# Performance work log

Measured on AMD Instinct MI355X. Metric: run time of the kernel, lower is better.

Reference implementation:

```python
import jax, jax.numpy as jnp
import numpy as np

N, E, DIM, H = 50000, 800000, 64, 2
HD = H * DIM


def setup_inputs() -> dict:
    key = jax.random.key(0)
    ks = jax.random.split(key, 16)
    s = 0.05
    return {
        "x": jax.random.normal(ks[0], (N, DIM), jnp.float32),
        "edge_index": jax.random.randint(ks[1], (2, E), 0, N, jnp.int64),
        "Wq": jax.random.normal(ks[2], (DIM, HD), jnp.float32) * s,
        "bq": jax.random.normal(ks[3], (HD,), jnp.float32) * s,
        "Wk": jax.random.normal(ks[4], (DIM, HD), jnp.float32) * s,
        "bk": jax.random.normal(ks[5], (HD,), jnp.float32) * s,
        "Wv": jax.random.normal(ks[6], (DIM, HD), jnp.float32) * s,
        "bv": jax.random.normal(ks[7], (HD,), jnp.float32) * s,
        "Wskip": jax.random.normal(ks[8], (DIM, HD), jnp.float32) * s,
        "bskip": jax.random.normal(ks[9], (HD,), jnp.float32) * s,
        "Wc": jax.random.normal(ks[10], (HD, DIM), jnp.float32) * s,
        "bc": jax.random.normal(ks[11], (DIM,), jnp.float32) * s,
        "gamma": jnp.ones((DIM,), jnp.float32),
        "beta": jnp.zeros((DIM,), jnp.float32),
    }


def reference(x, edge_index, Wq, bq, Wk, bk, Wv, bv, Wskip, bskip, Wc, bc, gamma, beta):
    src, dst = edge_index[0], edge_index[1]  # messages flow src -> dst
    # TransformerConv: per-head q/k/v projections, [N, H, D]
    q = (x @ Wq + bq).reshape(N, H, DIM)
    k = (x @ Wk + bk).reshape(N, H, DIM)
    v = (x @ Wv + bv).reshape(N, H, DIM)
    scale = 1.0 / np.sqrt(DIM).astype(np.float32)
    # edge-wise attention logits: [E, H]
    alpha = jnp.einsum('ehd,ehd->eh', q[dst], k[src]) * scale
    # segment softmax over incoming edges of each dst node (PyG softmax)
    amax = jax.ops.segment_max(alpha, dst, num_segments=N)
    a = jnp.exp(alpha - amax[dst])
    asum = jax.ops.segment_sum(a, dst, num_segments=N)
    a = a / (asum[dst] + 1e-16)
    # weighted scatter-aggregate of values: [N, H, D] -> concat heads
    out = jax.ops.segment_sum(a[:, :, None] * v[src], dst, num_segments=N)
    out = out.reshape(N, HD)
    # root/skip connection (root_weight=True default)
    out = out + (x @ Wskip + bskip)
    # concat linear: H*D -> dim
    out = out @ Wc + bc
    # pyg.LayerNorm default mode='graph': normalize over ALL nodes+features
    out = out - out.mean()
    out = out / (out.std() + 1e-5)  # std with unbiased=False (jnp default ddof=0)
    return out * gamma + beta
```

## Files before the change

### kernel.cpp

```cpp
#include <hip/hip_runtime.h>
#include <hip/hip_bf16.h>

#define N_NODES 50000
#define N_EDGES 800000
#define DIM 64
#define NHEAD 2
#define HD 128
#define NCOL 448
#define MAXDEG 64

#define NBIN 196
#define BCAP 6144
#define ACH 2048
#define BIN_BLKS 391

#define PREP_B 112
#define PROJ_B 782

#define QSCALE 0.18033688011112042f

typedef short bf16x8 __attribute__((ext_vector_type(8)));
typedef float f32x16 __attribute__((ext_vector_type(16)));
typedef float f32x2 __attribute__((ext_vector_type(2)));

__device__ __forceinline__ unsigned short f2bf(float f) {
    unsigned u = __float_as_uint(f);
    unsigned r = (u + 0x7fffu + ((u >> 16) & 1u)) >> 16;
    return (unsigned short)r;
}
__device__ __forceinline__ unsigned char f2fp8(float f) {
    int r = __builtin_amdgcn_cvt_pk_fp8_f32(f, f, 0, false);
    return (unsigned char)(r & 0xff);
}

__global__ __launch_bounds__(256) void k_pb(
    const int* __restrict__ ei,
    const float* __restrict__ Wq, const float* __restrict__ bq,
    const float* __restrict__ Wk, const float* __restrict__ bk,
    const float* __restrict__ Wv, const float* __restrict__ bv,
    const float* __restrict__ Wskip, const float* __restrict__ bskip,
    const float* __restrict__ Wc, const float* __restrict__ bc,
    unsigned short* __restrict__ WallT, float* __restrict__ ball,
    int* __restrict__ bincnt, unsigned* __restrict__ bins,
    double* __restrict__ stats)
{
    const int t = threadIdx.x;
    if (blockIdx.x < PREP_B) {
        int gid = blockIdx.x * 256 + t;
        if (gid == 0) { stats[0] = 0.0; stats[1] = 0.0; }
        const int j = gid >> 6;
        const int d = gid & 63;
        float w, bb;
        if (j < 128) {
            w = Wq[d * HD + j] * QSCALE;
            bb = bq[j] * QSCALE;
        } else if (j < 256) {
            int jj = j - 128;
            w = Wk[d * HD + jj];
            bb = bk[jj];
        } else if (j < 384) {
            int jj = j - 256;
            int h = jj >> 6, jc = jj & 63;
            float s = 0.f, sb = 0.f;
            for (int c = 0; c < 64; c++) {
                float wc = Wc[(h * 64 + c) * DIM + jc];
                s  += Wv[d * HD + h * 64 + c] * wc;
                sb += bv[h * 64 + c] * wc;
            }
            w = s; bb = sb;
        } else {
            int jj = j - 384;
            float s = 0.f, sb = bc[jj];
            for (int c = 0; c < HD; c++) {
                float wc = Wc[c * DIM + jj];
                s  += Wskip[d * HD + c] * wc;
                sb += bskip[c] * wc;
            }
            w = s; bb = sb;
        }
        WallT[gid] = f2bf(w);
        if (d == 0) ball[j] = bb;
        return;
    }
    __shared__ unsigned pk[ACH];
    __shared__ unsigned char bbn[ACH];
    __shared__ unsigned ord[ACH];
    __shared__ int hist[256];
    __shared__ int lofs[256];
    __shared__ int gbase[256];
    const int e0 = (blockIdx.x - PREP_B) * ACH;
    hist[t] = 0;
    __syncthreads();
    for (int i = t; i < ACH; i += 256) {
        int e = e0 + i;
        if (e < N_EDGES) {
            int src = ei[e];
            int d = ei[N_EDGES + e];
            int bin = d >> 8;
            pk[i] = (unsigned)(((d & 255) << 16) | src);
            bbn[i] = (unsigned char)bin;
            atomicAdd(&hist[bin], 1);
        } else {
            bbn[i] = 255;
        }
    }
    __syncthreads();
    int h = hist[t];
    lofs[t] = h;
    __syncthreads();
    for (int off = 1; off < 256; off <<= 1) {
        int add = (t >= off) ? lofs[t - off] : 0;
        __syncthreads();
        lofs[t] += add;
        __syncthreads();
    }
    int excl = lofs[t] - h;
    if (t < NBIN && h > 0) gbase[t] = atomicAdd(&bincnt[t], h);
    __syncthreads();
    lofs[t] = excl;
    hist[t] = 0;
    __syncthreads();
    for (int i = t; i < ACH; i += 256) {
        int bin = bbn[i];
        if (bin != 255) {
            int sl = atomicAdd(&hist[bin], 1);
            ord[lofs[bin] + sl] = pk[i];
        }
    }
    __syncthreads();
    const int w = t >> 6, lane = t & 63;
    for (int bin = w; bin < NBIN; bin += 4) {
        int cnt = hist[bin];
        int lo = lofs[bin];
        int gb = gbase[bin];
        for (int i = lane; i < cnt; i += 64) {
            int pos = gb + i;
            if (pos < BCAP) bins[(size_t)bin * BCAP + pos] = ord[lo + i];
        }
    }
}

__global__ __launch_bounds__(256) void k_ep(
    const float* __restrict__ x,
    const unsigned short* __restrict__ WallT, const float* __restrict__ ball,
    float* __restrict__ q, unsigned char* __restrict__ kv, float* __restrict__ skipc,
    const int* __restrict__ bincnt, const unsigned* __restrict__ bins,
    int* __restrict__ deg, unsigned short* __restrict__ elist)
{
    const int blk = blockIdx.x;
    const int t = threadIdx.x;
    if (blk >= PROJ_B) {
        const int bin = blk - PROJ_B;
        __shared__ int nodecnt[256];
        nodecnt[t] = 0;
        __syncthreads();
        int cnt = bincnt[bin]; if (cnt > BCAP) cnt = BCAP;
        const unsigned* bp = bins + (size_t)bin * BCAP;
        for (int i = t; i < cnt; i += 256) {
            unsigned p = bp[i];
            int local = p >> 16;
            int src = p & 0xffff;
            int sl = atomicAdd(&nodecnt[local], 1);
            if (sl < MAXDEG)
                elist[((size_t)((bin << 8) | local)) * MAXDEG + sl] = (unsigned short)src;
        }
        __syncthreads();
        int node = (bin << 8) + t;
        if (node < N_NODES) {
            int dgv = nodecnt[t];
            deg[node] = dgv > MAXDEG ? MAXDEG : dgv;
        }
        return;
    }
    const int w = t >> 6;
    const int lane = t & 63;
    const int col = lane & 31;
    const int khalf = lane >> 5;
    const int n0 = blk * 64 + (w >> 1) * 32;
    const int ct0 = (w & 1) * 7;
    const int rowbase = 4 * khalf;

    int nread = n0 + col; if (nread >= N_NODES) nread = N_NODES - 1;
    const float* ap = x + (size_t)nread * 64 + khalf * 8;
    bf16x8 afrag[4];
#pragma unroll
    for (int kk = 0; kk < 4; kk++) {
        float4 xa = *((const float4*)(ap + kk * 16));
        float4 xb4 = *((const float4*)(ap + kk * 16 + 4));
        bf16x8 f;
        f[0] = (short)f2bf(xa.x); f[1] = (short)f2bf(xa.y);
        f[2] = (short)f2bf(xa.z); f[3] = (short)f2bf(xa.w);
        f[4] = (short)f2bf(xb4.x); f[5] = (short)f2bf(xb4.y);
        f[6] = (short)f2bf(xb4.z); f[7] = (short)f2bf(xb4.w);
        afrag[kk] = f;
    }

    for (int tt = 0; tt < 7; tt++) {
        const int gc = (ct0 + tt) * 32 + col;
        const float b = ball[gc];
        f32x16 acc;
#pragma unroll
        for (int r = 0; r < 16; r++) acc[r] = b;
        const unsigned short* bp = WallT + (size_t)gc * 64 + khalf * 8;
#pragma unroll
        for (int kk = 0; kk < 4; kk++) {
            bf16x8 bfrag = *((const bf16x8*)(bp + kk * 16));
            acc = __builtin_amdgcn_mfma_f32_32x32x16_bf16(afrag[kk], bfrag, acc, 0, 0, 0);
        }
        if (gc < 128) {
#pragma unroll
            for (int r = 0; r < 16; r++) {
                int node = n0 + (r & 3) + 8 * (r >> 2) + rowbase;
                if (node < N_NODES) q[(size_t)node * HD + gc] = acc[r];
            }
        } else if (gc < 384) {
            int ch = gc - 128;
#pragma unroll
            for (int r = 0; r < 16; r++) {
                int node = n0 + (r & 3) + 8 * (r >> 2) + rowbase;
                if (node < N_NODES) kv[(size_t)node * 256 + ch] = f2fp8(acc[r]);
            }
        } else {
#pragma unroll
            for (int r = 0; r < 16; r++) {
                int node = n0 + (r & 3) + 8 * (r >> 2) + rowbase;
                if (node < N_NODES) skipc[(size_t)node * DIM + (gc - 384)] = acc[r];
            }
        }
    }
}

__global__ __launch_bounds__(256) void k_attn(
    const float* __restrict__ q, const unsigned char* __restrict__ kv,
    const float* __restrict__ skipc,
    const int* __restrict__ deg, const unsigned short* __restrict__ elist,
    float* __restrict__ out, float* __restrict__ parts)
{
    const int w = threadIdx.x >> 6;
    const int lane = threadIdx.x & 63;
    const int g = lane >> 3;
    const int j = lane & 7;
    const int n = blockIdx.x * 4 + w;
    const f32x2* qp = (const f32x2*)(q + (size_t)n * HD);
    f32x2 q0[4], q1[4];
#pragma unroll
    for (int i = 0; i < 4; i++) { q0[i] = qp[4 * j + i]; q1[i] = qp[32 + 4 * j + i]; }
    const int myE = elist[(size_t)n * MAXDEG + lane];
    f32x2 acc0[4], acc1[4];
#pragma unroll
    for (int i = 0; i < 4; i++) {
        acc0[i] = (f32x2){0.f, 0.f};
        acc1[i] = (f32x2){0.f, 0.f};
    }
    float l0 = 0.f, l1 = 0.f;
    int dg = deg[n]; if (dg > MAXDEG) dg = MAXDEG;
    for (int b0 = 0; b0 < dg; b0 += 16) {
        int iA = b0 + g, iB = b0 + 8 + g;
        bool vA = iA < dg, vB = iB < dg;
        int sA = __shfl(myE, vA ? iA : 0, 64);
        int sB = __shfl(myE, vB ? iB : 0, 64);
        const uint2* kpA = (const uint2*)(kv + (size_t)sA * 256);
        const uint2* kpB = (const uint2*)(kv + (size_t)sB * 256);
        uint2 KA0 = kpA[j],      KA1 = kpA[8 + j];
        uint2 VA0 = kpA[16 + j], VA1 = kpA[24 + j];
        uint2 KB0 = kpB[j],      KB1 = kpB[8 + j];
        uint2 VB0 = kpB[16 + j], VB1 = kpB[24 + j];
        f32x2 pa0 = q0[0] * __builtin_amdgcn_cvt_pk_f32_fp8(KA0.x, false);
        pa0 += q0[1] * __builtin_amdgcn_cvt_pk_f32_fp8(KA0.x, true);
        pa0 += q0[2] * __builtin_amdgcn_cvt_pk_f32_fp8(KA0.y, false);
        pa0 += q0[3] * __builtin_amdgcn_cvt_pk_f32_fp8(KA0.y, true);
        f32x2 pa1 = q1[0] * __builtin_amdgcn_cvt_pk_f32_fp8(KA1.x, false);
        pa1 += q1[1] * __builtin_amdgcn_cvt_pk_f32_fp8(KA1.x, true);
        pa1 += q1[2] * __builtin_amdgcn_cvt_pk_f32_fp8(KA1.y, false);
        pa1 += q1[3] * __builtin_amdgcn_cvt_pk_f32_fp8(KA1.y, true);
        float p0A = pa0[0] + pa0[1];
        float p1A = pa1[0] + pa1[1];
        f32x2 pb0 = q0[0] * __builtin_amdgcn_cvt_pk_f32_fp8(KB0.x, false);
        pb0 += q0[1] * __builtin_amdgcn_cvt_pk_f32_fp8(KB0.x, true);
        pb0 += q0[2] * __builtin_amdgcn_cvt_pk_f32_fp8(KB0.y, false);
        pb0 += q0[3] * __builtin_amdgcn_cvt_pk_f32_fp8(KB0.y, true);
        f32x2 pb1 = q1[0] * __builtin_amdgcn_cvt_pk_f32_fp8(KB1.x, false);
        pb1 += q1[1] * __builtin_amdgcn_cvt_pk_f32_fp8(KB1.x, true);
        pb1 += q1[2] * __builtin_amdgcn_cvt_pk_f32_fp8(KB1.y, false);
        pb1 += q1[3] * __builtin_amdgcn_cvt_pk_f32_fp8(KB1.y, true);
        float p0B = pb0[0] + pb0[1];
        float p1B = pb1[0] + pb1[1];
#pragma unroll
        for (int off = 1; off < 8; off <<= 1) {
            p0A += __shfl_xor(p0A, off, 64);
            p1A += __shfl_xor(p1A, off, 64);
            p0B += __shfl_xor(p0B, off, 64);
            p1B += __shfl_xor(p1B, off, 64);
        }
        float w0A = vA ? __builtin_amdgcn_exp2f(p0A) : 0.f;
        float w1A = vA ? __builtin_amdgcn_exp2f(p1A) : 0.f;
        float w0B = vB ? __builtin_amdgcn_exp2f(p0B) : 0.f;
        float w1B = vB ? __builtin_amdgcn_exp2f(p1B) : 0.f;
        l0 += w0A + w0B; l1 += w1A + w1B;
        f32x2 w0Av = {w0A, w0A}, w1Av = {w1A, w1A};
        f32x2 w0Bv = {w0B, w0B}, w1Bv = {w1B, w1B};
        acc0[0] += w0Av * __builtin_amdgcn_cvt_pk_f32_fp8(VA0.x, false);
        acc0[1] += w0Av * __builtin_amdgcn_cvt_pk_f32_fp8(VA0.x, true);
        acc0[2] += w0Av * __builtin_amdgcn_cvt_pk_f32_fp8(VA0.y, false);
        acc0[3] += w0Av * __builtin_amdgcn_cvt_pk_f32_fp8(VA0.y, true);
        acc1[0] += w1Av * __builtin_amdgcn_cvt_pk_f32_fp8(VA1.x, false);
        acc1[1] += w1Av * __builtin_amdgcn_cvt_pk_f32_fp8(VA1.x, true);
        acc1[2] += w1Av * __builtin_amdgcn_cvt_pk_f32_fp8(VA1.y, false);
        acc1[3] += w1Av * __builtin_amdgcn_cvt_pk_f32_fp8(VA1.y, true);
        acc0[0] += w0Bv * __builtin_amdgcn_cvt_pk_f32_fp8(VB0.x, false);
        acc0[1] += w0Bv * __builtin_amdgcn_cvt_pk_f32_fp8(VB0.x, true);
        acc0[2] += w0Bv * __builtin_amdgcn_cvt_pk_f32_fp8(VB0.y, false);
        acc0[3] += w0Bv * __builtin_amdgcn_cvt_pk_f32_fp8(VB0.y, true);
        acc1[0] += w1Bv * __builtin_amdgcn_cvt_pk_f32_fp8(VB1.x, false);
        acc1[1] += w1Bv * __builtin_amdgcn_cvt_pk_f32_fp8(VB1.x, true);
        acc1[2] += w1Bv * __builtin_amdgcn_cvt_pk_f32_fp8(VB1.y, false);
        acc1[3] += w1Bv * __builtin_amdgcn_cvt_pk_f32_fp8(VB1.y, true);
    }
    float* a0 = (float*)acc0;
    float* a1 = (float*)acc1;
#pragma unroll
    for (int off = 8; off < 64; off <<= 1) {
        l0 += __shfl_xor(l0, off, 64);
        l1 += __shfl_xor(l1, off, 64);
#pragma unroll
        for (int i = 0; i < 8; i++) {
            a0[i] += __shfl_xor(a0[i], off, 64);
            a1[i] += __shfl_xor(a1[i], off, 64);
        }
    }
    if (g == 0) {
        float inv0 = 1.f / (l0 + 1e-16f), inv1 = 1.f / (l1 + 1e-16f);
        const float4* sk = (const float4*)(skipc + (size_t)n * DIM);
        float4 sa = sk[2 * j], sb = sk[2 * j + 1];
        float o[8];
        o[0] = a0[0] * inv0 + a1[0] * inv1 + sa.x;
        o[1] = a0[1] * inv0 + a1[1] * inv1 + sa.y;
        o[2] = a0[2] * inv0 + a1[2] * inv1 + sa.z;
        o[3] = a0[3] * inv0 + a1[3] * inv1 + sa.w;
        o[4] = a0[4] * inv0 + a1[4] * inv1 + sb.x;
        o[5] = a0[5] * inv0 + a1[5] * inv1 + sb.y;
        o[6] = a0[6] * inv0 + a1[6] * inv1 + sb.z;
        o[7] = a0[7] * inv0 + a1[7] * inv1 + sb.w;
        float4 r0 = {o[0], o[1], o[2], o[3]}, r1 = {o[4], o[5], o[6], o[7]};
        float4* op = (float4*)(out + (size_t)n * DIM);
        op[2 * j] = r0; op[2 * j + 1] = r1;
        float s_ = 0.f, ss = 0.f;
#pragma unroll
        for (int i = 0; i < 8; i++) { s_ += o[i]; ss += o[i] * o[i]; }
#pragma unroll
        for (int off = 1; off < 8; off <<= 1) {
            s_ += __shfl_xor(s_, off, 64);
            ss += __shfl_xor(ss, off, 64);
        }
        if (j == 0) { parts[n] = s_; parts[N_NODES + n] = ss; }
    }
}

#define RED_BLOCKS 100
__global__ __launch_bounds__(256) void k_reduce(
    const float* __restrict__ parts, double* __restrict__ stats)
{
    double s = 0.0, ss = 0.0;
    for (int i = blockIdx.x * 256 + threadIdx.x; i < N_NODES; i += RED_BLOCKS * 256) {
        s  += (double)parts[i];
        ss += (double)parts[N_NODES + i];
    }
#pragma unroll
    for (int off = 32; off > 0; off >>= 1) {
        s  += __shfl_down(s, off);
        ss += __shfl_down(ss, off);
    }
    __shared__ double sdd[8];
    int wave = threadIdx.x >> 6;
    if ((threadIdx.x & 63) == 0) { sdd[wave * 2] = s; sdd[wave * 2 + 1] = ss; }
    __syncthreads();
    if (threadIdx.x == 0) {
        double S = 0.0, SS = 0.0;
        for (int w = 0; w < 4; w++) { S += sdd[w * 2]; SS += sdd[w * 2 + 1]; }
        atomicAdd(&stats[0], S);
        atomicAdd(&stats[1], SS);
    }
}

__global__ __launch_bounds__(256) void k_norm(
    float* __restrict__ out, const double* __restrict__ stats,
    const float* __restrict__ gamma, const float* __restrict__ beta)
{
    int i = blockIdx.x * 256 + threadIdx.x;
    if (i >= N_NODES * DIM / 4) return;
    const double cnt = (double)N_NODES * (double)DIM;
    double mean = stats[0] / cnt;
    double var  = stats[1] / cnt - mean * mean;
    if (var < 0.0) var = 0.0;
    float mf = (float)mean;
    float inv = 1.0f / ((float)sqrt(var) + 1e-5f);
    float4 v = ((const float4*)out)[i];
    float4 gv = ((const float4*)gamma)[i & 15];
    float4 bv2 = ((const float4*)beta)[i & 15];
    v.x = (v.x - mf) * inv * gv.x + bv2.x;
    v.y = (v.y - mf) * inv * gv.y + bv2.y;
    v.z = (v.z - mf) * inv * gv.z + bv2.z;
    v.w = (v.w - mf) * inv * gv.w + bv2.w;
    ((float4*)out)[i] = v;
}

extern "C" void kernel_launch(void* const* d_in, const int* in_sizes, int n_in,
                              void* d_out, int out_size, void* d_ws, size_t ws_size,
                              hipStream_t stream) {
    const float* x     = (const float*)d_in[0];
    const int*   ei    = (const int*)d_in[1];
    const float* Wq    = (const float*)d_in[2];
    const float* bq    = (const float*)d_in[3];
    const float* Wk    = (const float*)d_in[4];
    const float* bk    = (const float*)d_in[5];
    const float* Wv    = (const float*)d_in[6];
    const float* bv    = (const float*)d_in[7];
    const float* Wsk   = (const float*)d_in[8];
    const float* bsk   = (const float*)d_in[9];
    const float* Wc    = (const float*)d_in[10];
    const float* bc    = (const float*)d_in[11];
    const float* gamma = (const float*)d_in[12];
    const float* beta  = (const float*)d_in[13];
    float* out = (float*)d_out;

    float* ws = (float*)d_ws;
    const size_t NF = (size_t)N_NODES * HD;
    float* q = ws;
    unsigned char* kv = (unsigned char*)(ws + NF);
    float* skipc = (float*)(kv + (size_t)N_NODES * 256);
    unsigned short* WallT = (unsigned short*)(skipc + (size_t)N_NODES * DIM);
    float* ball   = (float*)(WallT + NCOL * 64);
    int* bincnt   = (int*)(ball + NCOL);
    unsigned* bins = (unsigned*)(bincnt + 256);
    int* deg      = (int*)(bins + (size_t)NBIN * BCAP);
    unsigned short* elist = (unsigned short*)(deg + N_NODES);
    float* parts  = (float*)(elist + (size_t)NBIN * 256 * MAXDEG);
    double* stats = (double*)(parts + (size_t)N_NODES * 2);

    hipMemsetAsync(bincnt, 0, NBIN * sizeof(int), stream);
    hipLaunchKernelGGL(k_pb, dim3(PREP_B + BIN_BLKS), dim3(256), 0, stream,
                       ei, Wq, bq, Wk, bk, Wv, bv, Wsk, bsk, Wc, bc,
                       WallT, ball, bincnt, bins, stats);
    hipLaunchKernelGGL(k_ep, dim3(PROJ_B + NBIN), dim3(256), 0, stream,
                       x, WallT, ball, q, kv, skipc, bincnt, bins, deg, elist);
    hipLaunchKernelGGL(k_attn, dim3(N_NODES / 4), dim3(256), 0, stream,
                       q, kv, skipc, deg, elist, out, parts);
    hipLaunchKernelGGL(k_reduce, dim3(RED_BLOCKS), dim3(256), 0, stream, parts, stats);
    hipLaunchKernelGGL(k_norm, dim3(N_NODES * DIM / 4 / 256 + 1), dim3(256), 0, stream,
                       out, stats, gamma, beta);
}
```

Measured before the change: 190.1 us.

## Replace two-pass binned edge bucketing with direct global-atomic adjacency build, interleave KV layout

The edge bucketing no longer sorts edges into bins in shared memory and then scatters them per bin in a second kernel. Each edge now does a global atomicAdd on its destination's degree and writes its source straight into that node's fixed-size adjacency slot. The K/V fp8 layout is interleaved so each lane fetches both heads' K and V with one 16-byte load per edge, and the attention loop now handles 8 edges per step instead of 16. The trade-off is many contended global atomics and scattered 2-byte writes in exchange for fewer kernel phases and no bin buffers. Degrees above MAXDEG are still clamped when read.

```diff
diff --git a/kernel.cpp b/kernel.cpp
--- a/kernel.cpp
+++ b/kernel.cpp
@@ -9,10 +9,8 @@
 #define NCOL 448
 #define MAXDEG 64
 
-#define NBIN 196
-#define BCAP 6144
 #define ACH 2048
-#define BIN_BLKS 391
+#define EDGE_BLKS 391
 
 #define PREP_B 112
 #define PROJ_B 782
@@ -41,7 +39,7 @@
     const float* __restrict__ Wskip, const float* __restrict__ bskip,
     const float* __restrict__ Wc, const float* __restrict__ bc,
     unsigned short* __restrict__ WallT, float* __restrict__ ball,
-    int* __restrict__ bincnt, unsigned* __restrict__ bins,
+    int* __restrict__ deg, unsigned short* __restrict__ elist,
     double* __restrict__ stats)
 {
     const int t = threadIdx.x;
@@ -82,60 +80,16 @@
         if (d == 0) ball[j] = bb;
         return;
     }
-    __shared__ unsigned pk[ACH];
-    __shared__ unsigned char bbn[ACH];
-    __shared__ unsigned ord[ACH];
-    __shared__ int hist[256];
-    __shared__ int lofs[256];
-    __shared__ int gbase[256];
     const int e0 = (blockIdx.x - PREP_B) * ACH;
-    hist[t] = 0;
-    __syncthreads();
+#pragma unroll 2
     for (int i = t; i < ACH; i += 256) {
         int e = e0 + i;
         if (e < N_EDGES) {
             int src = ei[e];
             int d = ei[N_EDGES + e];
-            int bin = d >> 8;
-            pk[i] = (unsigned)(((d & 255) << 16) | src);
-            bbn[i] = (unsigned char)bin;
-            atomicAdd(&hist[bin], 1);
-        } else {
-            bbn[i] = 255;
-        }
-    }
-    __syncthreads();
-    int h = hist[t];
-    lofs[t] = h;
-    __syncthreads();
-    for (int off = 1; off < 256; off <<= 1) {
-        int add = (t >= off) ? lofs[t - off] : 0;
-        __syncthreads();
-        lofs[t] += add;
-        __syncthreads();
-    }
-    int excl = lofs[t] - h;
-    if (t < NBIN && h > 0) gbase[t] = atomicAdd(&bincnt[t], h);
-    __syncthreads();
-    lofs[t] = excl;
-    hist[t] = 0;
-    __syncthreads();
-    for (int i = t; i < ACH; i += 256) {
-        int bin = bbn[i];
-        if (bin != 255) {
-            int sl = atomicAdd(&hist[bin], 1);
-            ord[lofs[bin] + sl] = pk[i];
-        }
-    }
-    __syncthreads();
-    const int w = t >> 6, lane = t & 63;
-    for (int bin = w; bin < NBIN; bin += 4) {
-        int cnt = hist[bin];
-        int lo = lofs[bin];
-        int gb = gbase[bin];
-        for (int i = lane; i < cnt; i += 64) {
-            int pos = gb + i;
-            if (pos < BCAP) bins[(size_t)bin * BCAP + pos] = ord[lo + i];
+            int sl = atomicAdd(&deg[d], 1);
+            if (sl < MAXDEG)
+                elist[(size_t)d * MAXDEG + sl] = (unsigned short)src;
         }
     }
 }
@@ -143,35 +97,10 @@
 __global__ __launch_bounds__(256) void k_ep(
     const float* __restrict__ x,
     const unsigned short* __restrict__ WallT, const float* __restrict__ ball,
-    float* __restrict__ q, unsigned char* __restrict__ kv, float* __restrict__ skipc,
-    const int* __restrict__ bincnt, const unsigned* __restrict__ bins,
-    int* __restrict__ deg, unsigned short* __restrict__ elist)
+    float* __restrict__ q, unsigned char* __restrict__ kv, float* __restrict__ skipc)
 {
     const int blk = blockIdx.x;
     const int t = threadIdx.x;
-    if (blk >= PROJ_B) {
-        const int bin = blk - PROJ_B;
-        __shared__ int nodecnt[256];
-        nodecnt[t] = 0;
-        __syncthreads();
-        int cnt = bincnt[bin]; if (cnt > BCAP) cnt = BCAP;
-        const unsigned* bp = bins + (size_t)bin * BCAP;
-        for (int i = t; i < cnt; i += 256) {
-            unsigned p = bp[i];
-            int local = p >> 16;
-            int src = p & 0xffff;
-            int sl = atomicAdd(&nodecnt[local], 1);
-            if (sl < MAXDEG)
-                elist[((size_t)((bin << 8) | local)) * MAXDEG + sl] = (unsigned short)src;
-        }
-        __syncthreads();
-        int node = (bin << 8) + t;
-        if (node < N_NODES) {
-            int dgv = nodecnt[t];
-            deg[node] = dgv > MAXDEG ? MAXDEG : dgv;
-        }
-        return;
-    }
     const int w = t >> 6;
     const int lane = t & 63;
     const int col = lane & 31;
@@ -215,10 +144,14 @@
             }
         } else if (gc < 384) {
             int ch = gc - 128;
+            int half = ch >> 7;
+            int cc = ch & 127;
+            int h = cc >> 6, c = cc & 63;
+            int pos = half * 128 + ((c >> 3) << 4) + (h << 3) + (c & 7);
 #pragma unroll
             for (int r = 0; r < 16; r++) {
                 int node = n0 + (r & 3) + 8 * (r >> 2) + rowbase;
-                if (node < N_NODES) kv[(size_t)node * 256 + ch] = f2fp8(acc[r]);
+                if (node < N_NODES) kv[(size_t)node * 256 + pos] = f2fp8(acc[r]);
             }
         } else {
 #pragma unroll
@@ -254,67 +187,40 @@
     }
     float l0 = 0.f, l1 = 0.f;
     int dg = deg[n]; if (dg > MAXDEG) dg = MAXDEG;
-    for (int b0 = 0; b0 < dg; b0 += 16) {
-        int iA = b0 + g, iB = b0 + 8 + g;
-        bool vA = iA < dg, vB = iB < dg;
-        int sA = __shfl(myE, vA ? iA : 0, 64);
-        int sB = __shfl(myE, vB ? iB : 0, 64);
-        const uint2* kpA = (const uint2*)(kv + (size_t)sA * 256);
-        const uint2* kpB = (const uint2*)(kv + (size_t)sB * 256);
-        uint2 KA0 = kpA[j],      KA1 = kpA[8 + j];
-        uint2 VA0 = kpA[16 + j], VA1 = kpA[24 + j];
-        uint2 KB0 = kpB[j],      KB1 = kpB[8 + j];
-        uint2 VB0 = kpB[16 + j], VB1 = kpB[24 + j];
-        f32x2 pa0 = q0[0] * __builtin_amdgcn_cvt_pk_f32_fp8(KA0.x, false);
-        pa0 += q0[1] * __builtin_amdgcn_cvt_pk_f32_fp8(KA0.x, true);
-        pa0 += q0[2] * __builtin_amdgcn_cvt_pk_f32_fp8(KA0.y, false);
-        pa0 += q0[3] * __builtin_amdgcn_cvt_pk_f32_fp8(KA0.y, true);
-        f32x2 pa1 = q1[0] * __builtin_amdgcn_cvt_pk_f32_fp8(KA1.x, false);
-        pa1 += q1[1] * __builtin_amdgcn_cvt_pk_f32_fp8(KA1.x, true);
-        pa1 += q1[2] * __builtin_amdgcn_cvt_pk_f32_fp8(KA1.y, false);
-        pa1 += q1[3] * __builtin_amdgcn_cvt_pk_f32_fp8(KA1.y, true);
-        float p0A = pa0[0] + pa0[1];
-        float p1A = pa1[0] + pa1[1];
-        f32x2 pb0 = q0[0] * __builtin_amdgcn_cvt_pk_f32_fp8(KB0.x, false);
-        pb0 += q0[1] * __builtin_amdgcn_cvt_pk_f32_fp8(KB0.x, true);
-        pb0 += q0[2] * __builtin_amdgcn_cvt_pk_f32_fp8(KB0.y, false);
-        pb0 += q0[3] * __builtin_amdgcn_cvt_pk_f32_fp8(KB0.y, true);
-        f32x2 pb1 = q1[0] * __builtin_amdgcn_cvt_pk_f32_fp8(KB1.x, false);
-        pb1 += q1[1] * __builtin_amdgcn_cvt_pk_f32_fp8(KB1.x, true);
-        pb1 += q1[2] * __builtin_amdgcn_cvt_pk_f32_fp8(KB1.y, false);
-        pb1 += q1[3] * __builtin_amdgcn_cvt_pk_f32_fp8(KB1.y, true);
-        float p0B = pb0[0] + pb0[1];
-        float p1B = pb1[0] + pb1[1];
+    for (int b0 = 0; b0 < dg; b0 += 8) {
+        int idx = b0 + g;
+        bool valid = idx < dg;
+        int s = __shfl(myE, valid ? idx : 0, 64);
+        const uint4* kp = (const uint4*)(kv + (size_t)s * 256);
+        uint4 K = kp[j];
+        uint4 V = kp[8 + j];
+        f32x2 p0v = q0[0] * __builtin_amdgcn_cvt_pk_f32_fp8(K.x, false);
+        p0v += q0[1] * __builtin_amdgcn_cvt_pk_f32_fp8(K.x, true);
+        p0v += q0[2] * __builtin_amdgcn_cvt_pk_f32_fp8(K.y, false);
+        p0v += q0[3] * __builtin_amdgcn_cvt_pk_f32_fp8(K.y, true);
+        f32x2 p1v = q1[0] * __builtin_amdgcn_cvt_pk_f32_fp8(K.z, false);
+        p1v += q1[1] * __builtin_amdgcn_cvt_pk_f32_fp8(K.z, true);
+        p1v += q1[2] * __builtin_amdgcn_cvt_pk_f32_fp8(K.w, false);
+        p1v += q1[3] * __builtin_amdgcn_cvt_pk_f32_fp8(K.w, true);
+        float p0 = p0v[0] + p0v[1];
+        float p1 = p1v[0] + p1v[1];
 #pragma unroll
         for (int off = 1; off < 8; off <<= 1) {
-            p0A += __shfl_xor(p0A, off, 64);
-            p1A += __shfl_xor(p1A, off, 64);
-            p0B += __shfl_xor(p0B, off, 64);
-            p1B += __shfl_xor(p1B, off, 64);
-        }
-        float w0A = vA ? __builtin_amdgcn_exp2f(p0A) : 0.f;
-        float w1A = vA ? __builtin_amdgcn_exp2f(p1A) : 0.f;
-        float w0B = vB ? __builtin_amdgcn_exp2f(p0B) : 0.f;
-        float w1B = vB ? __builtin_amdgcn_exp2f(p1B) : 0.f;
-        l0 += w0A + w0B; l1 += w1A + w1B;
-        f32x2 w0Av = {w0A, w0A}, w1Av = {w1A, w1A};
-        f32x2 w0Bv = {w0B, w0B}, w1Bv = {w1B, w1B};
-        acc0[0] += w0Av * __builtin_amdgcn_cvt_pk_f32_fp8(VA0.x, false);
-        acc0[1] += w0Av * __builtin_amdgcn_cvt_pk_f32_fp8(VA0.x, true);
-        acc0[2] += w0Av * __builtin_amdgcn_cvt_pk_f32_fp8(VA0.y, false);
-        acc0[3] += w0Av * __builtin_amdgcn_cvt_pk_f32_fp8(VA0.y, true);
-        acc1[0] += w1Av * __builtin_amdgcn_cvt_pk_f32_fp8(VA1.x, false);
-        acc1[1] += w1Av * __builtin_amdgcn_cvt_pk_f32_fp8(VA1.x, true);
-        acc1[2] += w1Av * __builtin_amdgcn_cvt_pk_f32_fp8(VA1.y, false);
-        acc1[3] += w1Av * __builtin_amdgcn_cvt_pk_f32_fp8(VA1.y, true);
-        acc0[0] += w0Bv * __builtin_amdgcn_cvt_pk_f32_fp8(VB0.x, false);
-        acc0[1] += w0Bv * __builtin_amdgcn_cvt_pk_f32_fp8(VB0.x, true);
-        acc0[2] += w0Bv * __builtin_amdgcn_cvt_pk_f32_fp8(VB0.y, false);
-        acc0[3] += w0Bv * __builtin_amdgcn_cvt_pk_f32_fp8(VB0.y, true);
-        acc1[0] += w1Bv * __builtin_amdgcn_cvt_pk_f32_fp8(VB1.x, false);
-        acc1[1] += w1Bv * __builtin_amdgcn_cvt_pk_f32_fp8(VB1.x, true);
-        acc1[2] += w1Bv * __builtin_amdgcn_cvt_pk_f32_fp8(VB1.y, false);
-        acc1[3] += w1Bv * __builtin_amdgcn_cvt_pk_f32_fp8(VB1.y, true);
+            p0 += __shfl_xor(p0, off, 64);
+            p1 += __shfl_xor(p1, off, 64);
+        }
+        float w0 = valid ? __builtin_amdgcn_exp2f(p0) : 0.f;
+        float w1 = valid ? __builtin_amdgcn_exp2f(p1) : 0.f;
+        l0 += w0; l1 += w1;
+        f32x2 w0v = {w0, w0}, w1v = {w1, w1};
+        acc0[0] += w0v * __builtin_amdgcn_cvt_pk_f32_fp8(V.x, false);
+        acc0[1] += w0v * __builtin_amdgcn_cvt_pk_f32_fp8(V.x, true);
+        acc0[2] += w0v * __builtin_amdgcn_cvt_pk_f32_fp8(V.y, false);
+        acc0[3] += w0v * __builtin_amdgcn_cvt_pk_f32_fp8(V.y, true);
+        acc1[0] += w1v * __builtin_amdgcn_cvt_pk_f32_fp8(V.z, false);
+        acc1[1] += w1v * __builtin_amdgcn_cvt_pk_f32_fp8(V.z, true);
+        acc1[2] += w1v * __builtin_amdgcn_cvt_pk_f32_fp8(V.w, false);
+        acc1[3] += w1v * __builtin_amdgcn_cvt_pk_f32_fp8(V.w, true);
     }
     float* a0 = (float*)acc0;
     float* a1 = (float*)acc1;
@@ -430,19 +336,17 @@
     float* skipc = (float*)(kv + (size_t)N_NODES * 256);
     unsigned short* WallT = (unsigned short*)(skipc + (size_t)N_NODES * DIM);
     float* ball   = (float*)(WallT + NCOL * 64);
-    int* bincnt   = (int*)(ball + NCOL);
-    unsigned* bins = (unsigned*)(bincnt + 256);
-    int* deg      = (int*)(bins + (size_t)NBIN * BCAP);
+    int* deg      = (int*)(ball + NCOL);
     unsigned short* elist = (unsigned short*)(deg + N_NODES);
-    float* parts  = (float*)(elist + (size_t)NBIN * 256 * MAXDEG);
+    float* parts  = (float*)(elist + (size_t)N_NODES * MAXDEG);
     double* stats = (double*)(parts + (size_t)N_NODES * 2);
 
-    hipMemsetAsync(bincnt, 0, NBIN * sizeof(int), stream);
-    hipLaunchKernelGGL(k_pb, dim3(PREP_B + BIN_BLKS), dim3(256), 0, stream,
+    hipMemsetAsync(deg, 0, N_NODES * sizeof(int), stream);
+    hipLaunchKernelGGL(k_pb, dim3(PREP_B + EDGE_BLKS), dim3(256), 0, stream,
                        ei, Wq, bq, Wk, bk, Wv, bv, Wsk, bsk, Wc, bc,
-                       WallT, ball, bincnt, bins, stats);
-    hipLaunchKernelGGL(k_ep, dim3(PROJ_B + NBIN), dim3(256), 0, stream,
-                       x, WallT, ball, q, kv, skipc, bincnt, bins, deg, elist);
+                       WallT, ball, deg, elist, stats);
+    hipLaunchKernelGGL(k_ep, dim3(PROJ_B), dim3(256), 0, stream,
+                       x, WallT, ball, q, kv, skipc);
     hipLaunchKernelGGL(k_attn, dim3(N_NODES / 4), dim3(256), 0, stream,
                        q, kv, skipc, deg, elist, out, parts);
     hipLaunchKernelGGL(k_reduce, dim3(RED_BLOCKS), dim3(256), 0, stream, parts, stats);
```

Measured after the change: 210.3 us. 1.11x slower.
